# Performance work log

Hardware: AMD Instinct MI355X
Metric: run time of the kernel (lower is better)

The kernel has to match this reference:

```python
import jax, jax.numpy as jnp
import numpy as np

B, C, N = 4, 256, 4096
CQ = C // 4

def setup_inputs() -> dict:
    key = jax.random.key(0)
    ks = jax.random.split(key, 8)
    inputs = jax.random.normal(ks[0], (B, C, N), dtype=jnp.float32)
    # Conv1d(kernel=1) == pointwise linear over channels: weight [out_c, in_c], bias [out_c]
    sc = 1.0 / np.sqrt(C)
    wq = jax.random.uniform(ks[1], (CQ, C), jnp.float32, -sc, sc)
    bq = jax.random.uniform(ks[2], (CQ,), jnp.float32, -sc, sc)
    wk = jax.random.uniform(ks[3], (CQ, C), jnp.float32, -sc, sc)
    bk = jax.random.uniform(ks[4], (CQ,), jnp.float32, -sc, sc)
    wv = jax.random.uniform(ks[5], (C, C), jnp.float32, -sc, sc)
    bv = jax.random.uniform(ks[6], (C,), jnp.float32, -sc, sc)
    gamma = jax.random.normal(ks[7], (1,), jnp.float32) * 0.1  # nonzero so attention path is exercised
    return {"inputs": inputs, "wq": wq, "bq": bq, "wk": wk, "bk": bk, "wv": wv, "bv": bv, "gamma": gamma}

def reference(inputs, wq, bq, wk, bk, wv, bv, gamma):
    # pointwise conv1d projections: [B,C,N] -> [B,out_c,N]
    q = jnp.einsum('oc,bcn->bon', wq, inputs) + bq[None, :, None]   # [B,CQ,N]
    k = jnp.einsum('oc,bcn->bon', wk, inputs) + bk[None, :, None]   # [B,CQ,N]
    v = jnp.einsum('oc,bcn->bon', wv, inputs) + bv[None, :, None]   # [B,C,N]
    # s = q^T k : [B,N,N] (no scaling, as in the source)
    s = jnp.einsum('bon,bom->bnm', q, k)
    beta = jax.nn.softmax(s, axis=-1)
    # o = v @ beta : [B,C,N]
    o = jnp.einsum('bcn,bnm->bcm', v, beta)
    return gamma * o + inputs
```

## Files before the change

kernel.cpp:

```cpp
#include <hip/hip_runtime.h>

#define NB   4
#define C_IN 256
#define CQD  64
#define NPT  4096
#define L2E  1.44269504088896f

typedef __attribute__((ext_vector_type(8))) short bf16x8;
typedef __attribute__((ext_vector_type(4))) float f32x4;
typedef unsigned short u16;
typedef unsigned int   u32;

#define EXP2F(x)      __builtin_amdgcn_exp2f(x)
#define MFMA32(A,B,C) __builtin_amdgcn_mfma_f32_16x16x32_bf16(A,B,C,0,0,0)

__device__ __forceinline__ u16 f2bf(float f) {
    u32 u = __float_as_uint(f);
    u += 0x7fff + ((u >> 16) & 1);
    return (u16)(u >> 16);
}
__device__ __forceinline__ u32 pack_trunc(float lo, float hi) {
    return __builtin_amdgcn_perm(__float_as_uint(hi), __float_as_uint(lo), 0x07060302u);
}


__global__ void prep_kernel(
    const float* __restrict__ wq, const float* __restrict__ bq,
    const float* __restrict__ wk, const float* __restrict__ bk,
    const float* __restrict__ wv, const float* __restrict__ bv,
    u16* __restrict__ wbf, float* __restrict__ bias)
{
    const int gid = blockIdx.x*256 + threadIdx.x;
    if (gid < 384*256) {
        const int r = gid >> 8, c = gid & 255;
        const float v = (r < 64) ? wq[r*256 + c]
                      : (r < 128) ? wk[(r-64)*256 + c]
                                  : wv[(r-128)*256 + c];
        const int go  = r >> 4, c16 = r & 15;
        const int kk  = c >> 5, qh  = (c >> 3) & 3, j = c & 7;
        wbf[((size_t)(go*8 + kk))*512 + (16*qh + c16)*8 + j] = f2bf(v);
    } else if (gid < 384*256 + 384) {
        const int r = gid - 384*256;
        bias[r] = (r < 64) ? bq[r] : (r < 128) ? bk[r-64] : bv[r-128];
    }
}

union ProjShared {
    u16 x_t[32][264];
    struct { u16 qk[32][136]; u16 vl[256][40]; } ep;
};

__global__ __launch_bounds__(256) void proj_kernel(
    const float* __restrict__ x, const u16* __restrict__ wbf,
    const float* __restrict__ bias,
    u16* __restrict__ qF, u16* __restrict__ kF, u16* __restrict__ vF)
{
    __shared__ ProjShared sh;

    const int t  = threadIdx.x;
    const int n0 = blockIdx.x * 32;
    const int b  = blockIdx.y;

    {
        const int ln = t & 31;
        const int cg = t >> 5;
        #pragma unroll
        for (int rr = 0; rr < 8; rr++) {
            const int c = 4*cg + 32*rr;
            const float f0 = x[((size_t)(b*C_IN + c+0))*NPT + n0 + ln];
            const float f1 = x[((size_t)(b*C_IN + c+1))*NPT + n0 + ln];
            const float f2 = x[((size_t)(b*C_IN + c+2))*NPT + n0 + ln];
            const float f3 = x[((size_t)(b*C_IN + c+3))*NPT + n0 + ln];
            ushort4 u4;
            u4.x = f2bf(f0); u4.y = f2bf(f1); u4.z = f2bf(f2); u4.w = f2bf(f3);
            *(ushort4*)&sh.x_t[ln][c] = u4;
        }
    }
    __syncthreads();

    const int w = t >> 6, l = t & 63, q = l >> 4, c16 = l & 15;

    f32x4 acc[6][2];
    #pragma unroll
    for (int ot = 0; ot < 6; ot++)
        #pragma unroll
        for (int nt = 0; nt < 2; nt++)
            acc[ot][nt] = (f32x4){0.f, 0.f, 0.f, 0.f};

    #pragma unroll
    for (int kk = 0; kk < 8; kk++) {
        const bf16x8 bf0 = *(const bf16x8*)&sh.x_t[c16     ][kk*32 + 8*q];
        const bf16x8 bf1 = *(const bf16x8*)&sh.x_t[16 + c16][kk*32 + 8*q];
        #pragma unroll
        for (int ot = 0; ot < 6; ot++) {
            const bf16x8 af = *(const bf16x8*)&wbf[((size_t)((4*ot + w)*8 + kk))*512 + l*8];
            acc[ot][0] = MFMA32(af, bf0, acc[ot][0]);
            acc[ot][1] = MFMA32(af, bf1, acc[ot][1]);
        }
    }
    __syncthreads();

    #pragma unroll
    for (int ot = 0; ot < 6; ot++) {
        const int T  = 4*ot + w;
        const int ob = 16*T + 4*q;
        float b0 = bias[ob+0], b1 = bias[ob+1], b2 = bias[ob+2], b3 = bias[ob+3];
        #pragma unroll
        for (int nt = 0; nt < 2; nt++) {
            const f32x4 a = acc[ot][nt];
            const float v0 = a[0]+b0, v1 = a[1]+b1, v2 = a[2]+b2, v3 = a[3]+b3;
            if (ot < 2) {
                uint2 u;
                u.x = (u32)f2bf(v0) | ((u32)f2bf(v1) << 16);
                u.y = (u32)f2bf(v2) | ((u32)f2bf(v3) << 16);
                *(uint2*)&sh.ep.qk[16*nt + c16][16*T + 4*q] = u;
            } else {
                const int cb = 16*T - 128 + 4*q;
                sh.ep.vl[cb+0][16*nt + c16] = f2bf(v0);
                sh.ep.vl[cb+1][16*nt + c16] = f2bf(v1);
                sh.ep.vl[cb+2][16*nt + c16] = f2bf(v2);
                sh.ep.vl[cb+3][16*nt + c16] = f2bf(v3);
            }
        }
    }
    __syncthreads();

    {
        const int n    = t >> 3;
        const int c    = t & 7;
        const int g    = (n0 + n) >> 4;
        const int lane = 16*(c & 3) + (n & 15);
        const size_t dq = ((size_t)(b*256 + g))*1024 + (size_t)(c >> 2)*512 + lane*8;
        *(uint4*)&qF[dq] = *(uint4*)&sh.ep.qk[n][8*c];
        *(uint4*)&kF[dq] = *(uint4*)&sh.ep.qk[n][64 + 8*c];
        const int cg   = t >> 4, c16v = t & 15;
        const int pg   = n0 >> 5;
        u16* vdst = &vF[(((size_t)(b*16 + cg))*128 + pg)*512 + c16v*8];
        #pragma unroll
        for (int j = 0; j < 4; j++)
            *(uint4*)&vdst[j*128] = *(uint4*)&sh.ep.vl[t][8*j];
    }
}

__global__ __launch_bounds__(512, 2) void attn_kernel(
    const u16* __restrict__ qF, const u16* __restrict__ kF, const u16* __restrict__ vF,
    const float* __restrict__ gamma,
    const float* __restrict__ x, float* __restrict__ out)
{
    __shared__ uint2 p_l[2][2176];
    __shared__ float zl[8][68];

    const int t = threadIdx.x;
    const int w = t >> 6, l = t & 63, q = l >> 4, c16 = l & 15;

    const int id  = blockIdx.x;
    const int xcd = id & 7;
    const int jb  = id >> 3;
    const int b   = xcd >> 1;
    const int ntt = ((xcd & 1) << 5) | jb;
    const int n0  = ntt * 64;

    bf16x8 qf[4][2];
    #pragma unroll
    for (int nj = 0; nj < 4; nj++) {
        const u16* qp = &qF[((size_t)(b*256 + ntt*4 + nj))*1024 + l*8];
        qf[nj][0] = *(const bf16x8*)qp;
        qf[nj][1] = *(const bf16x8*)(qp + 512);
    }

    f32x4 acc[2][4];
    #pragma unroll
    for (int cg = 0; cg < 2; cg++)
        #pragma unroll
        for (int nj = 0; nj < 4; nj++)
            acc[cg][nj] = (f32x4){0.f, 0.f, 0.f, 0.f};

    float zacc[4] = {0.f, 0.f, 0.f, 0.f};

    const u16* kbase  = &kF[((size_t)(b*256 + w))*1024 + l*8];
    const u16* vbase0 = &vF[(((size_t)(b*16 + 2*w))*128)*512 + l*8];
    const u16* vbase1 = vbase0 + (size_t)128*512;

    const int Uw  = (w*16 + q*4)*17 + c16;
    const int Ur0 = ((q>>1)*16 + (q&1)*8)*17 + c16;

    bf16x8 ka0 = *(const bf16x8*)kbase;
    bf16x8 ka1 = *(const bf16x8*)(kbase + 512);
    bf16x8 vac0[4], vac1[4];
    #pragma unroll
    for (int kc = 0; kc < 4; kc++) {
        vac0[kc] = *(const bf16x8*)(vbase0 + (size_t)kc*512);
        vac1[kc] = *(const bf16x8*)(vbase1 + (size_t)kc*512);
    }
    {
        f32x4 s[4];
        #pragma unroll
        for (int nj = 0; nj < 4; nj++) {
            f32x4 a = {0.f, 0.f, 0.f, 0.f};
            a = MFMA32(ka0, qf[nj][0], a);
            a = MFMA32(ka1, qf[nj][1], a);
            s[nj] = a;
        }
        #pragma unroll
        for (int nj = 0; nj < 4; nj++) {
            const float p0 = EXP2F(s[nj][0]*L2E);
            const float p1 = EXP2F(s[nj][1]*L2E);
            const float p2 = EXP2F(s[nj][2]*L2E);
            const float p3 = EXP2F(s[nj][3]*L2E);
            zacc[nj] += (p0 + p1) + (p2 + p3);
            uint2 u;
            u.x = pack_trunc(p0, p1);
            u.y = pack_trunc(p2, p3);
            p_l[0][Uw + nj*17] = u;
        }
    }
    ka0 = *(const bf16x8*)(kbase + 8192);
    ka1 = *(const bf16x8*)(kbase + 8192 + 512);

    int buf = 0;
    for (int mt = 0; mt < 31; mt++) {
        __syncthreads();
        f32x4 s[4];
        #pragma unroll
        for (int nj = 0; nj < 4; nj++) {
            f32x4 a = {0.f, 0.f, 0.f, 0.f};
            a = MFMA32(ka0, qf[nj][0], a);
            a = MFMA32(ka1, qf[nj][1], a);
            s[nj] = a;
        }
        #pragma unroll
        for (int nj = 0; nj < 4; nj++) {
            #pragma unroll
            for (int kc = 0; kc < 4; kc++) {
                const uint2 u0 = p_l[buf][Ur0 + kc*544 + nj*17];
                const uint2 u1 = p_l[buf][Ur0 + kc*544 + nj*17 + 68];
                uint4 f = make_uint4(u0.x, u0.y, u1.x, u1.y);
                const bf16x8 pf = *(bf16x8*)&f;
                acc[0][nj] = MFMA32(vac0[kc], pf, acc[0][nj]);
                acc[1][nj] = MFMA32(vac1[kc], pf, acc[1][nj]);
            }
        }
        const int m2 = (mt < 30) ? mt + 2 : 31;
        ka0 = *(const bf16x8*)(kbase + (size_t)m2*8192);
        ka1 = *(const bf16x8*)(kbase + (size_t)m2*8192 + 512);
        bf16x8 van0[4], van1[4];
        #pragma unroll
        for (int kc = 0; kc < 4; kc++) {
            van0[kc] = *(const bf16x8*)(vbase0 + (size_t)((mt+1)*4 + kc)*512);
            van1[kc] = *(const bf16x8*)(vbase1 + (size_t)((mt+1)*4 + kc)*512);
        }

        #pragma unroll
        for (int nj = 0; nj < 4; nj++) {
            const float p0 = EXP2F(s[nj][0]*L2E);
            const float p1 = EXP2F(s[nj][1]*L2E);
            const float p2 = EXP2F(s[nj][2]*L2E);
            const float p3 = EXP2F(s[nj][3]*L2E);
            zacc[nj] += (p0 + p1) + (p2 + p3);
            uint2 u;
            u.x = pack_trunc(p0, p1);
            u.y = pack_trunc(p2, p3);
            p_l[buf^1][Uw + nj*17] = u;
        }
        #pragma unroll
        for (int kc = 0; kc < 4; kc++) {
            vac0[kc] = van0[kc];
            vac1[kc] = van1[kc];
        }
        buf ^= 1;
    }
    __syncthreads();
    #pragma unroll
    for (int nj = 0; nj < 4; nj++) {
        #pragma unroll
        for (int kc = 0; kc < 4; kc++) {
            const uint2 u0 = p_l[buf][Ur0 + kc*544 + nj*17];
            const uint2 u1 = p_l[buf][Ur0 + kc*544 + nj*17 + 68];
            uint4 f = make_uint4(u0.x, u0.y, u1.x, u1.y);
            const bf16x8 pf = *(bf16x8*)&f;
            acc[0][nj] = MFMA32(vac0[kc], pf, acc[0][nj]);
            acc[1][nj] = MFMA32(vac1[kc], pf, acc[1][nj]);
        }
    }

    #pragma unroll
    for (int nj = 0; nj < 4; nj++) {
        zacc[nj] += __shfl_xor(zacc[nj], 16, 64);
        zacc[nj] += __shfl_xor(zacc[nj], 32, 64);
    }
    if (q == 0) {
        #pragma unroll
        for (int nj = 0; nj < 4; nj++) zl[w][16*nj + c16] = zacc[nj];
    }
    __syncthreads();

    float rz[4];
    #pragma unroll
    for (int nj = 0; nj < 4; nj++) {
        float zt = 0.f;
        #pragma unroll
        for (int w8 = 0; w8 < 8; w8++) zt += zl[w8][16*nj + c16];
        rz[nj] = 1.0f / zt;
    }

    const float g = gamma[0];
    #pragma unroll
    for (int cg = 0; cg < 2; cg++)
        #pragma unroll
        for (int nj = 0; nj < 4; nj++)
            #pragma unroll
            for (int r = 0; r < 4; r++) {
                const size_t o = ((size_t)(b*C_IN + 32*w + 16*cg + 4*q + r))*NPT
                               + n0 + 16*nj + c16;
                out[o] = g*(acc[cg][nj][r]*rz[nj]) + x[o];
            }
}

extern "C" void kernel_launch(void* const* d_in, const int* in_sizes, int n_in,
                              void* d_out, int out_size, void* d_ws, size_t ws_size,
                              hipStream_t stream)
{
    const float* x     = (const float*)d_in[0];
    const float* wq    = (const float*)d_in[1];
    const float* bq    = (const float*)d_in[2];
    const float* wk    = (const float*)d_in[3];
    const float* bk    = (const float*)d_in[4];
    const float* wv    = (const float*)d_in[5];
    const float* bv    = (const float*)d_in[6];
    const float* gamma = (const float*)d_in[7];
    float* out = (float*)d_out;

    u16* qF  = (u16*)d_ws;
    u16* kF  = qF  + (size_t)NB*NPT*CQD;
    u16* vF  = kF  + (size_t)NB*NPT*CQD;
    u16* wbf = vF  + (size_t)NB*C_IN*NPT;
    float* bias = (float*)(wbf + 384*256);

    prep_kernel<<<dim3(386), 256, 0, stream>>>(wq, bq, wk, bk, wv, bv, wbf, bias);
    proj_kernel<<<dim3(NPT/32, NB), 256, 0, stream>>>(x, wbf, bias, qF, kF, vF);
    attn_kernel<<<dim3(256), 512, 0, stream>>>(qF, kF, vF, gamma, x, out);
}
```

Baseline: 142.6 us.

## Repack P tile in LDS for 128-bit reads and reorder V loads

Changes the shared-memory layout of the probability tile from a padded stride-17 uint2 layout to an interleaved unpadded layout, so each MFMA B operand is read with one 128-bit LDS load instead of two 64-bit loads. V fragments are now loaded inside the iteration that uses them rather than prefetched one iteration ahead, which saves registers. The exp/pack/write of the next P tile is moved before the PV MFMAs. Dropping the padding may introduce LDS bank conflicts on the writes, and losing the V prefetch exposes more global-load latency inside each iteration.

```diff
diff --git a/kernel.cpp b/kernel.cpp
--- a/kernel.cpp
+++ b/kernel.cpp
@@ -147,7 +147,7 @@
     const float* __restrict__ gamma,
     const float* __restrict__ x, float* __restrict__ out)
 {
-    __shared__ uint2 p_l[2][2176];
+    __shared__ uint2 p2[2][2048];
     __shared__ float zl[8][68];
 
     const int t = threadIdx.x;
@@ -181,17 +181,12 @@
     const u16* vbase0 = &vF[(((size_t)(b*16 + 2*w))*128)*512 + l*8];
     const u16* vbase1 = vbase0 + (size_t)128*512;
 
-    const int Uw  = (w*16 + q*4)*17 + c16;
-    const int Ur0 = ((q>>1)*16 + (q&1)*8)*17 + c16;
+    const int g   = 4*w + q;
+    const int wb0 = (g>>1)*32 + c16*2 + (g&1);
+    const int rb0 = q*16 + c16;
 
     bf16x8 ka0 = *(const bf16x8*)kbase;
     bf16x8 ka1 = *(const bf16x8*)(kbase + 512);
-    bf16x8 vac0[4], vac1[4];
-    #pragma unroll
-    for (int kc = 0; kc < 4; kc++) {
-        vac0[kc] = *(const bf16x8*)(vbase0 + (size_t)kc*512);
-        vac1[kc] = *(const bf16x8*)(vbase1 + (size_t)kc*512);
-    }
     {
         f32x4 s[4];
         #pragma unroll
@@ -205,13 +200,13 @@
         for (int nj = 0; nj < 4; nj++) {
             const float p0 = EXP2F(s[nj][0]*L2E);
             const float p1 = EXP2F(s[nj][1]*L2E);
-            const float p2 = EXP2F(s[nj][2]*L2E);
+            const float p2v = EXP2F(s[nj][2]*L2E);
             const float p3 = EXP2F(s[nj][3]*L2E);
-            zacc[nj] += (p0 + p1) + (p2 + p3);
+            zacc[nj] += (p0 + p1) + (p2v + p3);
             uint2 u;
             u.x = pack_trunc(p0, p1);
-            u.y = pack_trunc(p2, p3);
-            p_l[0][Uw + nj*17] = u;
+            u.y = pack_trunc(p2v, p3);
+            p2[0][wb0 + nj*512] = u;
         }
     }
     ka0 = *(const bf16x8*)(kbase + 8192);
@@ -228,58 +223,60 @@
             a = MFMA32(ka1, qf[nj][1], a);
             s[nj] = a;
         }
-        #pragma unroll
-        for (int nj = 0; nj < 4; nj++) {
-            #pragma unroll
-            for (int kc = 0; kc < 4; kc++) {
-                const uint2 u0 = p_l[buf][Ur0 + kc*544 + nj*17];
-                const uint2 u1 = p_l[buf][Ur0 + kc*544 + nj*17 + 68];
-                uint4 f = make_uint4(u0.x, u0.y, u1.x, u1.y);
-                const bf16x8 pf = *(bf16x8*)&f;
-                acc[0][nj] = MFMA32(vac0[kc], pf, acc[0][nj]);
-                acc[1][nj] = MFMA32(vac1[kc], pf, acc[1][nj]);
-            }
+        bf16x8 va0[4], va1[4];
+        #pragma unroll
+        for (int kc = 0; kc < 4; kc++) {
+            va0[kc] = *(const bf16x8*)(vbase0 + (size_t)(mt*4 + kc)*512);
+            va1[kc] = *(const bf16x8*)(vbase1 + (size_t)(mt*4 + kc)*512);
         }
         const int m2 = (mt < 30) ? mt + 2 : 31;
         ka0 = *(const bf16x8*)(kbase + (size_t)m2*8192);
         ka1 = *(const bf16x8*)(kbase + (size_t)m2*8192 + 512);
-        bf16x8 van0[4], van1[4];
-        #pragma unroll
-        for (int kc = 0; kc < 4; kc++) {
-            van0[kc] = *(const bf16x8*)(vbase0 + (size_t)((mt+1)*4 + kc)*512);
-            van1[kc] = *(const bf16x8*)(vbase1 + (size_t)((mt+1)*4 + kc)*512);
-        }
 
         #pragma unroll
         for (int nj = 0; nj < 4; nj++) {
             const float p0 = EXP2F(s[nj][0]*L2E);
             const float p1 = EXP2F(s[nj][1]*L2E);
-            const float p2 = EXP2F(s[nj][2]*L2E);
+            const float p2v = EXP2F(s[nj][2]*L2E);
             const float p3 = EXP2F(s[nj][3]*L2E);
-            zacc[nj] += (p0 + p1) + (p2 + p3);
+            zacc[nj] += (p0 + p1) + (p2v + p3);
             uint2 u;
             u.x = pack_trunc(p0, p1);
-            u.y = pack_trunc(p2, p3);
-            p_l[buf^1][Uw + nj*17] = u;
-        }
+            u.y = pack_trunc(p2v, p3);
+            p2[buf^1][wb0 + nj*512] = u;
+        }
+
+        const uint4* pr = (const uint4*)p2[buf];
+        #pragma unroll
+        for (int nj = 0; nj < 4; nj++) {
+            #pragma unroll
+            for (int kc = 0; kc < 4; kc++) {
+                const uint4 f = pr[rb0 + nj*256 + kc*64];
+                const bf16x8 pf = *(const bf16x8*)&f;
+                acc[0][nj] = MFMA32(va0[kc], pf, acc[0][nj]);
+                acc[1][nj] = MFMA32(va1[kc], pf, acc[1][nj]);
+            }
+        }
+        buf ^= 1;
+    }
+    __syncthreads();
+    {
+        bf16x8 va0[4], va1[4];
         #pragma unroll
         for (int kc = 0; kc < 4; kc++) {
-            vac0[kc] = van0[kc];
-            vac1[kc] = van1[kc];
-        }
-        buf ^= 1;
-    }
-    __syncthreads();
-    #pragma unroll
-    for (int nj = 0; nj < 4; nj++) {
-        #pragma unroll
-        for (int kc = 0; kc < 4; kc++) {
-            const uint2 u0 = p_l[buf][Ur0 + kc*544 + nj*17];
-            const uint2 u1 = p_l[buf][Ur0 + kc*544 + nj*17 + 68];
-            uint4 f = make_uint4(u0.x, u0.y, u1.x, u1.y);
-            const bf16x8 pf = *(bf16x8*)&f;
-            acc[0][nj] = MFMA32(vac0[kc], pf, acc[0][nj]);
-            acc[1][nj] = MFMA32(vac1[kc], pf, acc[1][nj]);
+            va0[kc] = *(const bf16x8*)(vbase0 + (size_t)(31*4 + kc)*512);
+            va1[kc] = *(const bf16x8*)(vbase1 + (size_t)(31*4 + kc)*512);
+        }
+        const uint4* pr = (const uint4*)p2[buf];
+        #pragma unroll
+        for (int nj = 0; nj < 4; nj++) {
+            #pragma unroll
+            for (int kc = 0; kc < 4; kc++) {
+                const uint4 f = pr[rb0 + nj*256 + kc*64];
+                const bf16x8 pf = *(const bf16x8*)&f;
+                acc[0][nj] = MFMA32(va0[kc], pf, acc[0][nj]);
+                acc[1][nj] = MFMA32(va1[kc], pf, acc[1][nj]);
+            }
         }
     }
 
@@ -303,7 +300,7 @@
         rz[nj] = 1.0f / zt;
     }
 
-    const float g = gamma[0];
+    const float gm = gamma[0];
     #pragma unroll
     for (int cg = 0; cg < 2; cg++)
         #pragma unroll
@@ -312,7 +309,7 @@
             for (int r = 0; r < 4; r++) {
                 const size_t o = ((size_t)(b*C_IN + 32*w + 16*cg + 4*q + r))*NPT
                                + n0 + 16*nj + c16;
-                out[o] = g*(acc[cg][nj][r]*rz[nj]) + x[o];
+                out[o] = gm*(acc[cg][nj][r]*rz[nj]) + x[o];
             }
 }
 
```

Result: slower. 161.0 us (+12.9%).

## Fuse prep, projection and attention into one cooperative kernel with grid syncs

Applied to the files above, without the earlier changes.

Replaces the three separate launches (weight prep, QKV projection, attention) with a single cooperative kernel of 256 blocks of 512 threads, using grid.sync between phases. Each block handles two 256-thread projection tiles at once, then runs the same attention loop. This removes kernel launch gaps and tail effects between stages, at the cost of grid-wide barriers, dropped __restrict__ qualifiers, and launch bounds of (512,1) instead of (512,2), which may change register allocation for the attention phase.

```diff
diff --git a/kernel.cpp b/kernel.cpp
--- a/kernel.cpp
+++ b/kernel.cpp
@@ -1,4 +1,7 @@
 #include <hip/hip_runtime.h>
+#include <hip/hip_cooperative_groups.h>
+
+namespace cg = cooperative_groups;
 
 #define NB   4
 #define C_IN 256
@@ -24,210 +27,257 @@
 }
 
 
-__global__ void prep_kernel(
-    const float* __restrict__ wq, const float* __restrict__ bq,
-    const float* __restrict__ wk, const float* __restrict__ bk,
-    const float* __restrict__ wv, const float* __restrict__ bv,
-    u16* __restrict__ wbf, float* __restrict__ bias)
-{
-    const int gid = blockIdx.x*256 + threadIdx.x;
-    if (gid < 384*256) {
-        const int r = gid >> 8, c = gid & 255;
-        const float v = (r < 64) ? wq[r*256 + c]
-                      : (r < 128) ? wk[(r-64)*256 + c]
-                                  : wv[(r-128)*256 + c];
-        const int go  = r >> 4, c16 = r & 15;
-        const int kk  = c >> 5, qh  = (c >> 3) & 3, j = c & 7;
-        wbf[((size_t)(go*8 + kk))*512 + (16*qh + c16)*8 + j] = f2bf(v);
-    } else if (gid < 384*256 + 384) {
-        const int r = gid - 384*256;
-        bias[r] = (r < 64) ? bq[r] : (r < 128) ? bk[r-64] : bv[r-128];
-    }
-}
-
 union ProjShared {
     u16 x_t[32][264];
     struct { u16 qk[32][136]; u16 vl[256][40]; } ep;
 };
 
-__global__ __launch_bounds__(256) void proj_kernel(
-    const float* __restrict__ x, const u16* __restrict__ wbf,
-    const float* __restrict__ bias,
-    u16* __restrict__ qF, u16* __restrict__ kF, u16* __restrict__ vF)
+union FusedShared {
+    ProjShared proj[2];
+    struct { uint2 p_l[2][2176]; float zl[8][68]; } at;
+};
+
+__global__ __launch_bounds__(512, 1) void fused_kernel(
+    const float* x, const float* wq, const float* bq,
+    const float* wk, const float* bk, const float* wv, const float* bv,
+    const float* gamma, u16* wbf, float* bias,
+    u16* qF, u16* kF, u16* vF, float* out)
 {
-    __shared__ ProjShared sh;
-
-    const int t  = threadIdx.x;
-    const int n0 = blockIdx.x * 32;
-    const int b  = blockIdx.y;
+    __shared__ FusedShared fsh;
+    const int t = threadIdx.x;
+    cg::grid_group grid = cg::this_grid();
 
     {
-        const int ln = t & 31;
-        const int cg = t >> 5;
-        #pragma unroll
-        for (int rr = 0; rr < 8; rr++) {
-            const int c = 4*cg + 32*rr;
-            const float f0 = x[((size_t)(b*C_IN + c+0))*NPT + n0 + ln];
-            const float f1 = x[((size_t)(b*C_IN + c+1))*NPT + n0 + ln];
-            const float f2 = x[((size_t)(b*C_IN + c+2))*NPT + n0 + ln];
-            const float f3 = x[((size_t)(b*C_IN + c+3))*NPT + n0 + ln];
-            ushort4 u4;
-            u4.x = f2bf(f0); u4.y = f2bf(f1); u4.z = f2bf(f2); u4.w = f2bf(f3);
-            *(ushort4*)&sh.x_t[ln][c] = u4;
+        const int gid = blockIdx.x*512 + t;
+        if (gid < 384*256) {
+            const int r = gid >> 8, c = gid & 255;
+            const float v = (r < 64) ? wq[r*256 + c]
+                          : (r < 128) ? wk[(r-64)*256 + c]
+                                      : wv[(r-128)*256 + c];
+            const int go  = r >> 4, c16 = r & 15;
+            const int kk  = c >> 5, qh  = (c >> 3) & 3, j = c & 7;
+            wbf[((size_t)(go*8 + kk))*512 + (16*qh + c16)*8 + j] = f2bf(v);
+        } else if (gid < 384*256 + 384) {
+            const int r = gid - 384*256;
+            bias[r] = (r < 64) ? bq[r] : (r < 128) ? bk[r-64] : bv[r-128];
         }
     }
-    __syncthreads();
-
-    const int w = t >> 6, l = t & 63, q = l >> 4, c16 = l & 15;
-
-    f32x4 acc[6][2];
-    #pragma unroll
-    for (int ot = 0; ot < 6; ot++)
-        #pragma unroll
-        for (int nt = 0; nt < 2; nt++)
-            acc[ot][nt] = (f32x4){0.f, 0.f, 0.f, 0.f};
-
-    #pragma unroll
-    for (int kk = 0; kk < 8; kk++) {
-        const bf16x8 bf0 = *(const bf16x8*)&sh.x_t[c16     ][kk*32 + 8*q];
-        const bf16x8 bf1 = *(const bf16x8*)&sh.x_t[16 + c16][kk*32 + 8*q];
+    __threadfence();
+    grid.sync();
+
+    {
+        const int grp = t >> 8, tt = t & 255;
+        const int vb  = blockIdx.x*2 + grp;
+        const int n0  = (vb & 127) * 32;
+        const int b   = vb >> 7;
+        ProjShared& sh = fsh.proj[grp];
+
+        {
+            const int ln = tt & 31;
+            const int cg = tt >> 5;
+            #pragma unroll
+            for (int rr = 0; rr < 8; rr++) {
+                const int c = 4*cg + 32*rr;
+                const float f0 = x[((size_t)(b*C_IN + c+0))*NPT + n0 + ln];
+                const float f1 = x[((size_t)(b*C_IN + c+1))*NPT + n0 + ln];
+                const float f2 = x[((size_t)(b*C_IN + c+2))*NPT + n0 + ln];
+                const float f3 = x[((size_t)(b*C_IN + c+3))*NPT + n0 + ln];
+                ushort4 u4;
+                u4.x = f2bf(f0); u4.y = f2bf(f1); u4.z = f2bf(f2); u4.w = f2bf(f3);
+                *(ushort4*)&sh.x_t[ln][c] = u4;
+            }
+        }
+        __syncthreads();
+
+        const int w = tt >> 6, l = tt & 63, q = l >> 4, c16 = l & 15;
+
+        f32x4 acc[6][2];
+        #pragma unroll
+        for (int ot = 0; ot < 6; ot++)
+            #pragma unroll
+            for (int nt = 0; nt < 2; nt++)
+                acc[ot][nt] = (f32x4){0.f, 0.f, 0.f, 0.f};
+
+        #pragma unroll
+        for (int kk = 0; kk < 8; kk++) {
+            const bf16x8 bf0 = *(const bf16x8*)&sh.x_t[c16     ][kk*32 + 8*q];
+            const bf16x8 bf1 = *(const bf16x8*)&sh.x_t[16 + c16][kk*32 + 8*q];
+            #pragma unroll
+            for (int ot = 0; ot < 6; ot++) {
+                const bf16x8 af = *(const bf16x8*)&wbf[((size_t)((4*ot + w)*8 + kk))*512 + l*8];
+                acc[ot][0] = MFMA32(af, bf0, acc[ot][0]);
+                acc[ot][1] = MFMA32(af, bf1, acc[ot][1]);
+            }
+        }
+        __syncthreads();
+
         #pragma unroll
         for (int ot = 0; ot < 6; ot++) {
-            const bf16x8 af = *(const bf16x8*)&wbf[((size_t)((4*ot + w)*8 + kk))*512 + l*8];
-            acc[ot][0] = MFMA32(af, bf0, acc[ot][0]);
-            acc[ot][1] = MFMA32(af, bf1, acc[ot][1]);
+            const int T  = 4*ot + w;
+            const int ob = 16*T + 4*q;
+            float b0 = bias[ob+0], b1 = bias[ob+1], b2 = bias[ob+2], b3 = bias[ob+3];
+            #pragma unroll
+            for (int nt = 0; nt < 2; nt++) {
+                const f32x4 a = acc[ot][nt];
+                const float v0 = a[0]+b0, v1 = a[1]+b1, v2 = a[2]+b2, v3 = a[3]+b3;
+                if (ot < 2) {
+                    uint2 u;
+                    u.x = (u32)f2bf(v0) | ((u32)f2bf(v1) << 16);
+                    u.y = (u32)f2bf(v2) | ((u32)f2bf(v3) << 16);
+                    *(uint2*)&sh.ep.qk[16*nt + c16][16*T + 4*q] = u;
+                } else {
+                    const int cb = 16*T - 128 + 4*q;
+                    sh.ep.vl[cb+0][16*nt + c16] = f2bf(v0);
+                    sh.ep.vl[cb+1][16*nt + c16] = f2bf(v1);
+                    sh.ep.vl[cb+2][16*nt + c16] = f2bf(v2);
+                    sh.ep.vl[cb+3][16*nt + c16] = f2bf(v3);
+                }
+            }
+        }
+        __syncthreads();
+
+        {
+            const int n    = tt >> 3;
+            const int c    = tt & 7;
+            const int g    = (n0 + n) >> 4;
+            const int lane = 16*(c & 3) + (n & 15);
+            const size_t dq = ((size_t)(b*256 + g))*1024 + (size_t)(c >> 2)*512 + lane*8;
+            *(uint4*)&qF[dq] = *(uint4*)&sh.ep.qk[n][8*c];
+            *(uint4*)&kF[dq] = *(uint4*)&sh.ep.qk[n][64 + 8*c];
+            const int cg   = tt >> 4, c16v = tt & 15;
+            const int pg   = n0 >> 5;
+            u16* vdst = &vF[(((size_t)(b*16 + cg))*128 + pg)*512 + c16v*8];
+            #pragma unroll
+            for (int j = 0; j < 4; j++)
+                *(uint4*)&vdst[j*128] = *(uint4*)&sh.ep.vl[tt][8*j];
         }
     }
-    __syncthreads();
-
-    #pragma unroll
-    for (int ot = 0; ot < 6; ot++) {
-        const int T  = 4*ot + w;
-        const int ob = 16*T + 4*q;
-        float b0 = bias[ob+0], b1 = bias[ob+1], b2 = bias[ob+2], b3 = bias[ob+3];
-        #pragma unroll
-        for (int nt = 0; nt < 2; nt++) {
-            const f32x4 a = acc[ot][nt];
-            const float v0 = a[0]+b0, v1 = a[1]+b1, v2 = a[2]+b2, v3 = a[3]+b3;
-            if (ot < 2) {
+    __threadfence();
+    grid.sync();
+
+    {
+        auto& p_l = fsh.at.p_l;
+        auto& zl  = fsh.at.zl;
+
+        const int w = t >> 6, l = t & 63, q = l >> 4, c16 = l & 15;
+
+        const int id  = blockIdx.x;
+        const int xcd = id & 7;
+        const int jb  = id >> 3;
+        const int b   = xcd >> 1;
+        const int ntt = ((xcd & 1) << 5) | jb;
+        const int n0  = ntt * 64;
+
+        bf16x8 qf[4][2];
+        #pragma unroll
+        for (int nj = 0; nj < 4; nj++) {
+            const u16* qp = &qF[((size_t)(b*256 + ntt*4 + nj))*1024 + l*8];
+            qf[nj][0] = *(const bf16x8*)qp;
+            qf[nj][1] = *(const bf16x8*)(qp + 512);
+        }
+
+        f32x4 acc[2][4];
+        #pragma unroll
+        for (int cg = 0; cg < 2; cg++)
+            #pragma unroll
+            for (int nj = 0; nj < 4; nj++)
+                acc[cg][nj] = (f32x4){0.f, 0.f, 0.f, 0.f};
+
+        float zacc[4] = {0.f, 0.f, 0.f, 0.f};
+
+        const u16* kbase  = &kF[((size_t)(b*256 + w))*1024 + l*8];
+        const u16* vbase0 = &vF[(((size_t)(b*16 + 2*w))*128)*512 + l*8];
+        const u16* vbase1 = vbase0 + (size_t)128*512;
+
+        const int Uw  = (w*16 + q*4)*17 + c16;
+        const int Ur0 = ((q>>1)*16 + (q&1)*8)*17 + c16;
+
+        bf16x8 ka0 = *(const bf16x8*)kbase;
+        bf16x8 ka1 = *(const bf16x8*)(kbase + 512);
+        bf16x8 vac0[4], vac1[4];
+        #pragma unroll
+        for (int kc = 0; kc < 4; kc++) {
+            vac0[kc] = *(const bf16x8*)(vbase0 + (size_t)kc*512);
+            vac1[kc] = *(const bf16x8*)(vbase1 + (size_t)kc*512);
+        }
+        {
+            f32x4 s[4];
+            #pragma unroll
+            for (int nj = 0; nj < 4; nj++) {
+                f32x4 a = {0.f, 0.f, 0.f, 0.f};
+                a = MFMA32(ka0, qf[nj][0], a);
+                a = MFMA32(ka1, qf[nj][1], a);
+                s[nj] = a;
+            }
+            #pragma unroll
+            for (int nj = 0; nj < 4; nj++) {
+                const float p0 = EXP2F(s[nj][0]*L2E);
+                const float p1 = EXP2F(s[nj][1]*L2E);
+                const float p2 = EXP2F(s[nj][2]*L2E);
+                const float p3 = EXP2F(s[nj][3]*L2E);
+                zacc[nj] += (p0 + p1) + (p2 + p3);
                 uint2 u;
-                u.x = (u32)f2bf(v0) | ((u32)f2bf(v1) << 16);
-                u.y = (u32)f2bf(v2) | ((u32)f2bf(v3) << 16);
-                *(uint2*)&sh.ep.qk[16*nt + c16][16*T + 4*q] = u;
-            } else {
-                const int cb = 16*T - 128 + 4*q;
-                sh.ep.vl[cb+0][16*nt + c16] = f2bf(v0);
-                sh.ep.vl[cb+1][16*nt + c16] = f2bf(v1);
-                sh.ep.vl[cb+2][16*nt + c16] = f2bf(v2);
-                sh.ep.vl[cb+3][16*nt + c16] = f2bf(v3);
-            }
-        }
-    }
-    __syncthreads();
-
-    {
-        const int n    = t >> 3;
-        const int c    = t & 7;
-        const int g    = (n0 + n) >> 4;
-        const int lane = 16*(c & 3) + (n & 15);
-        const size_t dq = ((size_t)(b*256 + g))*1024 + (size_t)(c >> 2)*512 + lane*8;
-        *(uint4*)&qF[dq] = *(uint4*)&sh.ep.qk[n][8*c];
-        *(uint4*)&kF[dq] = *(uint4*)&sh.ep.qk[n][64 + 8*c];
-        const int cg   = t >> 4, c16v = t & 15;
-        const int pg   = n0 >> 5;
-        u16* vdst = &vF[(((size_t)(b*16 + cg))*128 + pg)*512 + c16v*8];
-        #pragma unroll
-        for (int j = 0; j < 4; j++)
-            *(uint4*)&vdst[j*128] = *(uint4*)&sh.ep.vl[t][8*j];
-    }
-}
-
-__global__ __launch_bounds__(512, 2) void attn_kernel(
-    const u16* __restrict__ qF, const u16* __restrict__ kF, const u16* __restrict__ vF,
-    const float* __restrict__ gamma,
-    const float* __restrict__ x, float* __restrict__ out)
-{
-    __shared__ uint2 p_l[2][2176];
-    __shared__ float zl[8][68];
-
-    const int t = threadIdx.x;
-    const int w = t >> 6, l = t & 63, q = l >> 4, c16 = l & 15;
-
-    const int id  = blockIdx.x;
-    const int xcd = id & 7;
-    const int jb  = id >> 3;
-    const int b   = xcd >> 1;
-    const int ntt = ((xcd & 1) << 5) | jb;
-    const int n0  = ntt * 64;
-
-    bf16x8 qf[4][2];
-    #pragma unroll
-    for (int nj = 0; nj < 4; nj++) {
-        const u16* qp = &qF[((size_t)(b*256 + ntt*4 + nj))*1024 + l*8];
-        qf[nj][0] = *(const bf16x8*)qp;
-        qf[nj][1] = *(const bf16x8*)(qp + 512);
-    }
-
-    f32x4 acc[2][4];
-    #pragma unroll
-    for (int cg = 0; cg < 2; cg++)
-        #pragma unroll
-        for (int nj = 0; nj < 4; nj++)
-            acc[cg][nj] = (f32x4){0.f, 0.f, 0.f, 0.f};
-
-    float zacc[4] = {0.f, 0.f, 0.f, 0.f};
-
-    const u16* kbase  = &kF[((size_t)(b*256 + w))*1024 + l*8];
-    const u16* vbase0 = &vF[(((size_t)(b*16 + 2*w))*128)*512 + l*8];
-    const u16* vbase1 = vbase0 + (size_t)128*512;
-
-    const int Uw  = (w*16 + q*4)*17 + c16;
-    const int Ur0 = ((q>>1)*16 + (q&1)*8)*17 + c16;
-
-    bf16x8 ka0 = *(const bf16x8*)kbase;
-    bf16x8 ka1 = *(const bf16x8*)(kbase + 512);
-    bf16x8 vac0[4], vac1[4];
-    #pragma unroll
-    for (int kc = 0; kc < 4; kc++) {
-        vac0[kc] = *(const bf16x8*)(vbase0 + (size_t)kc*512);
-        vac1[kc] = *(const bf16x8*)(vbase1 + (size_t)kc*512);
-    }
-    {
-        f32x4 s[4];
-        #pragma unroll
-        for (int nj = 0; nj < 4; nj++) {
-            f32x4 a = {0.f, 0.f, 0.f, 0.f};
-            a = MFMA32(ka0, qf[nj][0], a);
-            a = MFMA32(ka1, qf[nj][1], a);
-            s[nj] = a;
-        }
-        #pragma unroll
-        for (int nj = 0; nj < 4; nj++) {
-            const float p0 = EXP2F(s[nj][0]*L2E);
-            const float p1 = EXP2F(s[nj][1]*L2E);
-            const float p2 = EXP2F(s[nj][2]*L2E);
-            const float p3 = EXP2F(s[nj][3]*L2E);
-            zacc[nj] += (p0 + p1) + (p2 + p3);
-            uint2 u;
-            u.x = pack_trunc(p0, p1);
-            u.y = pack_trunc(p2, p3);
-            p_l[0][Uw + nj*17] = u;
-        }
-    }
-    ka0 = *(const bf16x8*)(kbase + 8192);
-    ka1 = *(const bf16x8*)(kbase + 8192 + 512);
-
-    int buf = 0;
-    for (int mt = 0; mt < 31; mt++) {
-        __syncthreads();
-        f32x4 s[4];
-        #pragma unroll
-        for (int nj = 0; nj < 4; nj++) {
-            f32x4 a = {0.f, 0.f, 0.f, 0.f};
-            a = MFMA32(ka0, qf[nj][0], a);
-            a = MFMA32(ka1, qf[nj][1], a);
-            s[nj] = a;
-        }
+                u.x = pack_trunc(p0, p1);
+                u.y = pack_trunc(p2, p3);
+                p_l[0][Uw + nj*17] = u;
+            }
+        }
+        ka0 = *(const bf16x8*)(kbase + 8192);
+        ka1 = *(const bf16x8*)(kbase + 8192 + 512);
+
+        int buf = 0;
+        for (int mt = 0; mt < 31; mt++) {
+            __syncthreads();
+            f32x4 s[4];
+            #pragma unroll
+            for (int nj = 0; nj < 4; nj++) {
+                f32x4 a = {0.f, 0.f, 0.f, 0.f};
+                a = MFMA32(ka0, qf[nj][0], a);
+                a = MFMA32(ka1, qf[nj][1], a);
+                s[nj] = a;
+            }
+            #pragma unroll
+            for (int nj = 0; nj < 4; nj++) {
+                #pragma unroll
+                for (int kc = 0; kc < 4; kc++) {
+                    const uint2 u0 = p_l[buf][Ur0 + kc*544 + nj*17];
+                    const uint2 u1 = p_l[buf][Ur0 + kc*544 + nj*17 + 68];
+                    uint4 f = make_uint4(u0.x, u0.y, u1.x, u1.y);
+                    const bf16x8 pf = *(bf16x8*)&f;
+                    acc[0][nj] = MFMA32(vac0[kc], pf, acc[0][nj]);
+                    acc[1][nj] = MFMA32(vac1[kc], pf, acc[1][nj]);
+                }
+            }
+            const int m2 = (mt < 30) ? mt + 2 : 31;
+            ka0 = *(const bf16x8*)(kbase + (size_t)m2*8192);
+            ka1 = *(const bf16x8*)(kbase + (size_t)m2*8192 + 512);
+            bf16x8 van0[4], van1[4];
+            #pragma unroll
+            for (int kc = 0; kc < 4; kc++) {
+                van0[kc] = *(const bf16x8*)(vbase0 + (size_t)((mt+1)*4 + kc)*512);
+                van1[kc] = *(const bf16x8*)(vbase1 + (size_t)((mt+1)*4 + kc)*512);
+            }
+
+            #pragma unroll
+            for (int nj = 0; nj < 4; nj++) {
+                const float p0 = EXP2F(s[nj][0]*L2E);
+                const float p1 = EXP2F(s[nj][1]*L2E);
+                const float p2 = EXP2F(s[nj][2]*L2E);
+                const float p3 = EXP2F(s[nj][3]*L2E);
+                zacc[nj] += (p0 + p1) + (p2 + p3);
+                uint2 u;
+                u.x = pack_trunc(p0, p1);
+                u.y = pack_trunc(p2, p3);
+                p_l[buf^1][Uw + nj*17] = u;
+            }
+            #pragma unroll
+            for (int kc = 0; kc < 4; kc++) {
+                vac0[kc] = van0[kc];
+                vac1[kc] = van1[kc];
+            }
+            buf ^= 1;
+        }
+        __syncthreads();
         #pragma unroll
         for (int nj = 0; nj < 4; nj++) {
             #pragma unroll
@@ -240,80 +290,39 @@
                 acc[1][nj] = MFMA32(vac1[kc], pf, acc[1][nj]);
             }
         }
-        const int m2 = (mt < 30) ? mt + 2 : 31;
-        ka0 = *(const bf16x8*)(kbase + (size_t)m2*8192);
-        ka1 = *(const bf16x8*)(kbase + (size_t)m2*8192 + 512);
-        bf16x8 van0[4], van1[4];
-        #pragma unroll
-        for (int kc = 0; kc < 4; kc++) {
-            van0[kc] = *(const bf16x8*)(vbase0 + (size_t)((mt+1)*4 + kc)*512);
-            van1[kc] = *(const bf16x8*)(vbase1 + (size_t)((mt+1)*4 + kc)*512);
-        }
 
         #pragma unroll
         for (int nj = 0; nj < 4; nj++) {
-            const float p0 = EXP2F(s[nj][0]*L2E);
-            const float p1 = EXP2F(s[nj][1]*L2E);
-            const float p2 = EXP2F(s[nj][2]*L2E);
-            const float p3 = EXP2F(s[nj][3]*L2E);
-            zacc[nj] += (p0 + p1) + (p2 + p3);
-            uint2 u;
-            u.x = pack_trunc(p0, p1);
-            u.y = pack_trunc(p2, p3);
-            p_l[buf^1][Uw + nj*17] = u;
-        }
-        #pragma unroll
-        for (int kc = 0; kc < 4; kc++) {
-            vac0[kc] = van0[kc];
-            vac1[kc] = van1[kc];
-        }
-        buf ^= 1;
+            zacc[nj] += __shfl_xor(zacc[nj], 16, 64);
+            zacc[nj] += __shfl_xor(zacc[nj], 32, 64);
+        }
+        if (q == 0) {
+            #pragma unroll
+            for (int nj = 0; nj < 4; nj++) zl[w][16*nj + c16] = zacc[nj];
+        }
+        __syncthreads();
+
+        float rz[4];
+        #pragma unroll
+        for (int nj = 0; nj < 4; nj++) {
+            float zt = 0.f;
+            #pragma unroll
+            for (int w8 = 0; w8 < 8; w8++) zt += zl[w8][16*nj + c16];
+            rz[nj] = 1.0f / zt;
+        }
+
+        const float gm = gamma[0];
+        #pragma unroll
+        for (int cg = 0; cg < 2; cg++)
+            #pragma unroll
+            for (int nj = 0; nj < 4; nj++)
+                #pragma unroll
+                for (int r = 0; r < 4; r++) {
+                    const size_t o = ((size_t)(b*C_IN + 32*w + 16*cg + 4*q + r))*NPT
+                                   + n0 + 16*nj + c16;
+                    out[o] = gm*(acc[cg][nj][r]*rz[nj]) + x[o];
+                }
     }
-    __syncthreads();
-    #pragma unroll
-    for (int nj = 0; nj < 4; nj++) {
-        #pragma unroll
-        for (int kc = 0; kc < 4; kc++) {
-            const uint2 u0 = p_l[buf][Ur0 + kc*544 + nj*17];
-            const uint2 u1 = p_l[buf][Ur0 + kc*544 + nj*17 + 68];
-            uint4 f = make_uint4(u0.x, u0.y, u1.x, u1.y);
-            const bf16x8 pf = *(bf16x8*)&f;
-            acc[0][nj] = MFMA32(vac0[kc], pf, acc[0][nj]);
-            acc[1][nj] = MFMA32(vac1[kc], pf, acc[1][nj]);
-        }
-    }
-
-    #pragma unroll
-    for (int nj = 0; nj < 4; nj++) {
-        zacc[nj] += __shfl_xor(zacc[nj], 16, 64);
-        zacc[nj] += __shfl_xor(zacc[nj], 32, 64);
-    }
-    if (q == 0) {
-        #pragma unroll
-        for (int nj = 0; nj < 4; nj++) zl[w][16*nj + c16] = zacc[nj];
-    }
-    __syncthreads();
-
-    float rz[4];
-    #pragma unroll
-    for (int nj = 0; nj < 4; nj++) {
-        float zt = 0.f;
-        #pragma unroll
-        for (int w8 = 0; w8 < 8; w8++) zt += zl[w8][16*nj + c16];
-        rz[nj] = 1.0f / zt;
-    }
-
-    const float g = gamma[0];
-    #pragma unroll
-    for (int cg = 0; cg < 2; cg++)
-        #pragma unroll
-        for (int nj = 0; nj < 4; nj++)
-            #pragma unroll
-            for (int r = 0; r < 4; r++) {
-                const size_t o = ((size_t)(b*C_IN + 32*w + 16*cg + 4*q + r))*NPT
-                               + n0 + 16*nj + c16;
-                out[o] = g*(acc[cg][nj][r]*rz[nj]) + x[o];
-            }
 }
 
 extern "C" void kernel_launch(void* const* d_in, const int* in_sizes, int n_in,
@@ -336,7 +345,11 @@
     u16* wbf = vF  + (size_t)NB*C_IN*NPT;
     float* bias = (float*)(wbf + 384*256);
 
-    prep_kernel<<<dim3(386), 256, 0, stream>>>(wq, bq, wk, bk, wv, bv, wbf, bias);
-    proj_kernel<<<dim3(NPT/32, NB), 256, 0, stream>>>(x, wbf, bias, qF, kF, vF);
-    attn_kernel<<<dim3(256), 512, 0, stream>>>(qF, kF, vF, gamma, x, out);
+    void* args[] = {
+        (void*)&x, (void*)&wq, (void*)&bq, (void*)&wk, (void*)&bk,
+        (void*)&wv, (void*)&bv, (void*)&gamma, (void*)&wbf, (void*)&bias,
+        (void*)&qF, (void*)&kF, (void*)&vF, (void*)&out
+    };
+    hipLaunchCooperativeKernel((const void*)fused_kernel,
+                               dim3(256), dim3(512), args, 0, stream);
 }
```

Measured after the change: 315.8 us. 2.21x slower.
